# Performance work log

Hardware: AMD Instinct MI355X
Metric: run time of the kernel (lower is better)

Reference implementation:

```python
import jax, jax.numpy as jnp
import numpy as np

N = 100000   # number of website nodes
E = 800000   # edges per edge type
F = 128      # in_feats == out_feats
NEG_SLOPE = 0.2


def setup_inputs() -> dict:
    key = jax.random.key(0)
    ks = jax.random.split(key, 16)
    s = 1.0 / np.sqrt(F)
    return {
        "feat": jax.random.normal(ks[0], (N, F), jnp.float32),
        "src_u": jax.random.randint(ks[1], (E,), 0, N),
        "dst_u": jax.random.randint(ks[2], (E,), 0, N),
        "src_r": jax.random.randint(ks[3], (E,), 0, N),
        "dst_r": jax.random.randint(ks[4], (E,), 0, N),
        # fc_self (no bias)
        "W_self": jax.random.uniform(ks[5], (F, F), jnp.float32, -s, s),
        # attn branch 'user'
        "W_u": jax.random.uniform(ks[6], (F, F), jnp.float32, -s, s),
        "a_l_u": jax.random.uniform(ks[7], (F,), jnp.float32, -s, s),
        "a_r_u": jax.random.uniform(ks[8], (F,), jnp.float32, -s, s),
        # attn branch 'reuse'
        "W_r": jax.random.uniform(ks[9], (F, F), jnp.float32, -s, s),
        "a_l_r": jax.random.uniform(ks[10], (F,), jnp.float32, -s, s),
        "a_r_r": jax.random.uniform(ks[11], (F,), jnp.float32, -s, s),
        # fc_neigh (with bias)
        "W_neigh": jax.random.uniform(ks[12], (F, F), jnp.float32, -s, s),
        "b_neigh": jax.random.uniform(ks[13], (F,), jnp.float32, -s, s),
        # module-level bias parameter
        "bias": jnp.zeros((F,), jnp.float32),
    }


def _attn_aggregate(feat, W, a_l, a_r, src, dst, n_nodes):
    """GAT-style single-head aggregation over one edge type.
    Returns [n_nodes, F] = sum_{e: dst(e)=v} softmax_v(leaky_relu(el[src]+er[dst])) * h[src]."""
    h = feat @ W                                    # [N, F] (feat_src == feat_dst)
    el = h @ a_l                                    # [N]
    er = h @ a_r                                    # [N]
    e = jax.nn.leaky_relu(el[src] + er[dst], NEG_SLOPE)   # [E]
    # edge_softmax: normalize over incoming edges of each dst node
    m = jax.ops.segment_max(e, dst, num_segments=n_nodes)  # [N] (-inf for isolated dst, unused)
    ex = jnp.exp(e - m[dst])                        # [E]
    denom = jax.ops.segment_sum(ex, dst, num_segments=n_nodes)  # [N]
    a = ex / denom[dst]                             # [E]
    msg = h[src] * a[:, None]                       # [E, F]
    return jax.ops.segment_sum(msg, dst, num_segments=n_nodes)  # [N, F]


def reference(feat, src_u, dst_u, src_r, dst_r, W_self, W_u, a_l_u, a_r_u,
              W_r, a_l_r, a_r_r, W_neigh, b_neigh, bias):
    n = feat.shape[0]
    neigh_u = _attn_aggregate(feat, W_u, a_l_u, a_r_u, src_u, dst_u, n)
    neigh_r = _attn_aggregate(feat, W_r, a_l_r, a_r_r, src_r, dst_r, n)
    # multi_update_all cross reducer 'mean' over the two edge types
    neigh = 0.5 * (neigh_u + neigh_r)
    h_neigh = neigh @ W_neigh + b_neigh             # fc_neigh
    rst = feat @ W_self + h_neigh                   # fc_self(h_self) + h_neigh
    return rst + bias
```

## Files before the change

### kernel.cpp

```cpp
#include <hip/hip_runtime.h>

#define F 128
#define NEG_SLOPE 0.2f
#define SHIFT 9
#define BPB 512
#define NBS 512

typedef _Float16 f16_t;
typedef _Float16 f16x8 __attribute__((ext_vector_type(8)));
typedef _Float16 f16x2 __attribute__((ext_vector_type(2)));
typedef float f32x4 __attribute__((ext_vector_type(4)));

__global__ __launch_bounds__(128) void prep_mats(
    const float* __restrict__ Wu, const float* __restrict__ Wr,
    const float* __restrict__ Ws, const float* __restrict__ Wn,
    const float* __restrict__ alu, const float* __restrict__ aru,
    const float* __restrict__ alr, const float* __restrict__ arr_,
    f16_t* __restrict__ Mtu, f16_t* __restrict__ Mtr, f16_t* __restrict__ Wts,
    float* __restrict__ wlu, float* __restrict__ wru,
    float* __restrict__ wlr, float* __restrict__ wrr)
{
    int b = blockIdx.x;
    int tid = threadIdx.x;
    if (b < 256) {
        int k = b & 127;
        const float* W = (b < 128) ? Wu : Wr;
        f16_t* M = (b < 128) ? Mtu : Mtr;
        float acc = 0.f;
        for (int t = 0; t < F; t++) acc += W[k * F + t] * Wn[t * F + tid];
        M[tid * F + k] = (f16_t)acc;
    } else if (b < 384) {
        int c = b - 256;
        Wts[c * F + tid] = (f16_t)Ws[tid * F + c];
    } else {
        int which = b - 384;
        const float* W = (which < 2) ? Wu : Wr;
        const float* a = (which == 0) ? alu : (which == 1) ? aru : (which == 2) ? alr : arr_;
        float acc = 0.f;
        for (int c = 0; c < F; c++) acc += W[tid * F + c] * a[c];
        float* o = (which == 0) ? wlu : (which == 1) ? wru : (which == 2) ? wlr : wrr;
        o[tid] = acc;
    }
}


__global__ __launch_bounds__(256) void cast_p1a(
    const float* __restrict__ feat,
    const float* __restrict__ wlu, const float* __restrict__ wru,
    const float* __restrict__ wlr, const float* __restrict__ wrr,
    f16_t* __restrict__ featb,
    float* __restrict__ elu, float* __restrict__ eru,
    float* __restrict__ elr, float* __restrict__ err_,
    const int* __restrict__ dst_u, const int* __restrict__ dst_r,
    int* __restrict__ cnt_bb,
    int Eu, int Et, int N, int chunk, int n, int nbk)
{
    int b = blockIdx.x;
    int tid = threadIdx.x;
    if (b < 256) {
        __shared__ int hist[NBS];
        for (int i = tid; i < NBS; i += 256) hist[i] = 0;
        __syncthreads();
        int e0 = b * chunk;
        int e1 = e0 + chunk; if (e1 > Et) e1 = Et;
        int u1 = (e1 < Eu) ? e1 : Eu;
        for (int e = e0 + tid; e < u1; e += 256) {
            int bin = dst_u[e];
            atomicAdd(&hist[bin >> SHIFT], 1);
        }
        int r0 = (e0 > Eu) ? e0 : Eu;
        for (int e = r0 + tid; e < e1; e += 256) {
            int bin = N + dst_r[e - Eu];
            atomicAdd(&hist[bin >> SHIFT], 1);
        }
        __syncthreads();
        for (int i = tid; i < NBS; i += 256) cnt_bb[b * NBS + i] = hist[i];
        return;
    }
    int fid = b - 256;
    int lane = tid & 63;
    int wave = tid >> 6;
    int lo = lane & 15, hi = lane >> 4;
    int base = fid * 64 + wave * 16;
    if (base >= n) return;
    int row = base + lo;
    if (row > n - 1) row = n - 1;
    const float* fp = feat + (size_t)row * F + hi * 8;
    f16_t* fb = featb + (size_t)row * F + hi * 8;
    const float* wsel = (lo == 0) ? wlu : (lo == 1) ? wru : (lo == 2) ? wlr : wrr;

    f32x4 acc = (f32x4){0.f, 0.f, 0.f, 0.f};
#pragma unroll
    for (int ks = 0; ks < 4; ks++) {
        float4 a0 = *(const float4*)(fp + ks * 32);
        float4 a1 = *(const float4*)(fp + ks * 32 + 4);
        f16x8 af;
        af[0] = (f16_t)a0.x; af[1] = (f16_t)a0.y; af[2] = (f16_t)a0.z; af[3] = (f16_t)a0.w;
        af[4] = (f16_t)a1.x; af[5] = (f16_t)a1.y; af[6] = (f16_t)a1.z; af[7] = (f16_t)a1.w;
        *(f16x8*)(fb + ks * 32) = af;
        f16x8 bf;
#pragma unroll
        for (int q = 0; q < 8; q++) bf[q] = (f16_t)0;
        if (lo < 4) {
            float4 b0 = *(const float4*)(wsel + ks * 32 + hi * 8);
            float4 b1 = *(const float4*)(wsel + ks * 32 + hi * 8 + 4);
            bf[0] = (f16_t)b0.x; bf[1] = (f16_t)b0.y; bf[2] = (f16_t)b0.z; bf[3] = (f16_t)b0.w;
            bf[4] = (f16_t)b1.x; bf[5] = (f16_t)b1.y; bf[6] = (f16_t)b1.z; bf[7] = (f16_t)b1.w;
        }
        acc = __builtin_amdgcn_mfma_f32_16x16x32_f16(af, bf, acc, 0, 0, 0);
    }
    if (lo < 4) {
        float* oarr = (lo == 0) ? elu : (lo == 1) ? eru : (lo == 2) ? elr : err_;
#pragma unroll
        for (int j = 0; j < 4; j++) {
            int r = base + hi * 4 + j;
            if (r < n) oarr[r] = acc[j];
        }
    }
}


__global__ __launch_bounds__(256) void scan_bb1(int* __restrict__ cnt_bb,
                                                int* __restrict__ btot, int nbk)
{
    int k = blockIdx.x;
    int tid = threadIdx.x;
    __shared__ int lds[256];
    int v = cnt_bb[tid * NBS + k];
    lds[tid] = v;
    __syncthreads();
    for (int off = 1; off < 256; off <<= 1) {
        int add = (tid >= off) ? lds[tid - off] : 0;
        __syncthreads();
        lds[tid] += add;
        __syncthreads();
    }
    cnt_bb[tid * NBS + k] = lds[tid] - v;
    if (tid == 255) btot[k] = lds[255];
}

__global__ __launch_bounds__(512) void scan_bb2(const int* __restrict__ btot,
                                                int* __restrict__ bbase,
                                                int* __restrict__ rp,
                                                int nbk, int twoN, int Et)
{
    __shared__ int lds[512];
    int t = threadIdx.x;
    int v = (t < nbk) ? btot[t] : 0;
    lds[t] = v;
    __syncthreads();
    for (int off = 1; off < 512; off <<= 1) {
        int add = (t >= off) ? lds[t - off] : 0;
        __syncthreads();
        lds[t] += add;
        __syncthreads();
    }
    bbase[t] = lds[t] - v;
    if (t == 0) rp[twoN] = Et;
}


__global__ __launch_bounds__(256) void p1b_scatter(
    const int* __restrict__ src_u, const int* __restrict__ dst_u,
    const int* __restrict__ src_r, const int* __restrict__ dst_r,
    const int* __restrict__ cnt_bb, const int* __restrict__ bbase,
    uint2* __restrict__ bucketed,
    int Eu, int Et, int N, int chunk, int nbk)
{
    int b = blockIdx.x;
    int tid = threadIdx.x;
    __shared__ int cur[NBS];
    for (int i = tid; i < nbk; i += 256) cur[i] = bbase[i] + cnt_bb[b * NBS + i];
    __syncthreads();
    int e0 = b * chunk;
    int e1 = e0 + chunk; if (e1 > Et) e1 = Et;
    int u1 = (e1 < Eu) ? e1 : Eu;
    for (int e = e0 + tid; e < u1; e += 256) {
        int bin = dst_u[e];
        int s = src_u[e];
        int pos = atomicAdd(&cur[bin >> SHIFT], 1);
        bucketed[pos] = make_uint2((unsigned)s, (unsigned)bin);
    }
    int r0 = (e0 > Eu) ? e0 : Eu;
    for (int e = r0 + tid; e < e1; e += 256) {
        int bin = N + dst_r[e - Eu];
        int s = src_r[e - Eu];
        int pos = atomicAdd(&cur[bin >> SHIFT], 1);
        bucketed[pos] = make_uint2((unsigned)s, (unsigned)bin);
    }
}


__global__ __launch_bounds__(256) void p2_build(
    const uint2* __restrict__ bucketed, const int* __restrict__ bbase,
    int* __restrict__ rp, int* __restrict__ csr, int twoN)
{
    int k = blockIdx.x;
    int tid = threadIdx.x;
    int beg = bbase[k], end = bbase[k + 1];
    __shared__ int hist[BPB];
    __shared__ int psum[256];
    for (int i = tid; i < BPB; i += 256) hist[i] = 0;
    __syncthreads();
    for (int i = beg + tid; i < end; i += 256) {
        uint2 p = bucketed[i];
        atomicAdd(&hist[p.y & (BPB - 1)], 1);
    }
    __syncthreads();
    int a0 = hist[2 * tid], a1 = hist[2 * tid + 1];
    psum[tid] = a0 + a1;
    __syncthreads();
    for (int off = 1; off < 256; off <<= 1) {
        int add = (tid >= off) ? psum[tid - off] : 0;
        __syncthreads();
        psum[tid] += add;
        __syncthreads();
    }
    int base0 = beg + psum[tid] - (a0 + a1);
    int bin0 = (k << SHIFT) + 2 * tid;
    if (bin0 < twoN)     rp[bin0]     = base0;
    if (bin0 + 1 < twoN) rp[bin0 + 1] = base0 + a0;
    __syncthreads();
    hist[2 * tid]     = base0;
    hist[2 * tid + 1] = base0 + a0;
    __syncthreads();
    for (int i = beg + tid; i < end; i += 256) {
        uint2 p = bucketed[i];
        int pos = atomicAdd(&hist[p.y & (BPB - 1)], 1);
        csr[pos] = (int)p.x;
    }
}


__global__ __launch_bounds__(256) void aggregate_fused(
    const f16_t* __restrict__ featb,
    const float* __restrict__ elu, const float* __restrict__ eru,
    const float* __restrict__ elr, const float* __restrict__ err_,
    const int* __restrict__ rp, const int* __restrict__ csr,
    f16_t* __restrict__ aggu, f16_t* __restrict__ aggr, int n)
{
    int wid = (int)(((size_t)blockIdx.x * 256 + threadIdx.x) >> 6);
    if (wid >= n) return;
    int lane = threadIdx.x & 63;
    int g = lane >> 4, lo = lane & 15;

    int begu = rp[wid],     endu = rp[wid + 1];
    int begr = rp[n + wid], endr = rp[n + wid + 1];
    float ervu = eru[wid];
    float ervr = err_[wid];

    union UP { f16x2 h; int i; };
    union UV { f16x8 v; f16x2 p[4]; };

    f16x2 z = {(f16_t)0, (f16_t)0};
    f16x2 au0 = z, au1 = z, au2 = z, au3 = z;
    f16x2 ar0 = z, ar1 = z, ar2 = z, ar3 = z;
    float du = 0.f, dr = 0.f;

    int iu = begu + g, ir = begr + g;

    int cu0 = (iu     < endu) ? csr[iu]     : -1;
    int cu1 = (iu + 4 < endu) ? csr[iu + 4] : -1;
    int cr0 = (ir     < endr) ? csr[ir]     : -1;
    int cr1 = (ir + 4 < endr) ? csr[ir + 4] : -1;
    UV hu0, hu1, hr0, hr1;
    hu0.v = *(const f16x8*)&featb[(size_t)(cu0 < 0 ? 0 : cu0) * F + lo * 8];
    hu1.v = *(const f16x8*)&featb[(size_t)(cu1 < 0 ? 0 : cu1) * F + lo * 8];
    hr0.v = *(const f16x8*)&featb[(size_t)(cr0 < 0 ? 0 : cr0) * F + lo * 8];
    hr1.v = *(const f16x8*)&featb[(size_t)(cr1 < 0 ? 0 : cr1) * F + lo * 8];
    float eu0 = elu[cu0 < 0 ? 0 : cu0];
    float eu1 = elu[cu1 < 0 ? 0 : cu1];
    float er0 = elr[cr0 < 0 ? 0 : cr0];
    float er1 = elr[cr1 < 0 ? 0 : cr1];

    while (iu < endu || ir < endr) {
        int nu0 = (iu + 8  < endu) ? csr[iu + 8]  : -1;
        int nu1 = (iu + 12 < endu) ? csr[iu + 12] : -1;
        int nr0 = (ir + 8  < endr) ? csr[ir + 8]  : -1;
        int nr1 = (ir + 12 < endr) ? csr[ir + 12] : -1;
        UV pu0, pu1, pr0, pr1;
        pu0.v = *(const f16x8*)&featb[(size_t)(nu0 < 0 ? 0 : nu0) * F + lo * 8];
        pu1.v = *(const f16x8*)&featb[(size_t)(nu1 < 0 ? 0 : nu1) * F + lo * 8];
        pr0.v = *(const f16x8*)&featb[(size_t)(nr0 < 0 ? 0 : nr0) * F + lo * 8];
        pr1.v = *(const f16x8*)&featb[(size_t)(nr1 < 0 ? 0 : nr1) * F + lo * 8];
        float fu0 = elu[nu0 < 0 ? 0 : nu0];
        float fu1 = elu[nu1 < 0 ? 0 : nu1];
        float fr0 = elr[nr0 < 0 ? 0 : nr0];
        float fr1 = elr[nr1 < 0 ? 0 : nr1];

        {
            float e = eu0 + ervu; e = fmaxf(e, NEG_SLOPE * e);
            float ex = (cu0 >= 0) ? __expf(e) : 0.f;
            f16_t exh = (f16_t)ex; f16x2 exv = {exh, exh};
            au0 += exv * hu0.p[0]; au1 += exv * hu0.p[1];
            au2 += exv * hu0.p[2]; au3 += exv * hu0.p[3];
            du += ex;
        }
        {
            float e = eu1 + ervu; e = fmaxf(e, NEG_SLOPE * e);
            float ex = (cu1 >= 0) ? __expf(e) : 0.f;
            f16_t exh = (f16_t)ex; f16x2 exv = {exh, exh};
            au0 += exv * hu1.p[0]; au1 += exv * hu1.p[1];
            au2 += exv * hu1.p[2]; au3 += exv * hu1.p[3];
            du += ex;
        }
        {
            float e = er0 + ervr; e = fmaxf(e, NEG_SLOPE * e);
            float ex = (cr0 >= 0) ? __expf(e) : 0.f;
            f16_t exh = (f16_t)ex; f16x2 exv = {exh, exh};
            ar0 += exv * hr0.p[0]; ar1 += exv * hr0.p[1];
            ar2 += exv * hr0.p[2]; ar3 += exv * hr0.p[3];
            dr += ex;
        }
        {
            float e = er1 + ervr; e = fmaxf(e, NEG_SLOPE * e);
            float ex = (cr1 >= 0) ? __expf(e) : 0.f;
            f16_t exh = (f16_t)ex; f16x2 exv = {exh, exh};
            ar0 += exv * hr1.p[0]; ar1 += exv * hr1.p[1];
            ar2 += exv * hr1.p[2]; ar3 += exv * hr1.p[3];
            dr += ex;
        }

        hu0 = pu0; hu1 = pu1; hr0 = pr0; hr1 = pr1;
        eu0 = fu0; eu1 = fu1; er0 = fr0; er1 = fr1;
        cu0 = nu0; cu1 = nu1; cr0 = nr0; cr1 = nr1;
        iu += 8; ir += 8;
    }

#pragma unroll
    for (int off = 16; off < 64; off <<= 1) {
        du += __shfl_xor(du, off);
        dr += __shfl_xor(dr, off);
        UP x;
        x.h = au0; x.i = __shfl_xor(x.i, off); au0 += x.h;
        x.h = au1; x.i = __shfl_xor(x.i, off); au1 += x.h;
        x.h = au2; x.i = __shfl_xor(x.i, off); au2 += x.h;
        x.h = au3; x.i = __shfl_xor(x.i, off); au3 += x.h;
        x.h = ar0; x.i = __shfl_xor(x.i, off); ar0 += x.h;
        x.h = ar1; x.i = __shfl_xor(x.i, off); ar1 += x.h;
        x.h = ar2; x.i = __shfl_xor(x.i, off); ar2 += x.h;
        x.h = ar3; x.i = __shfl_xor(x.i, off); ar3 += x.h;
    }

    if (g == 0) {
        float invu = (du > 0.f) ? 0.5f / du : 0.f;
        float invr = (dr > 0.f) ? 0.5f / dr : 0.f;
        f16_t ihu = (f16_t)invu, ihr = (f16_t)invr;
        f16x2 ivu = {ihu, ihu}, ivr = {ihr, ihr};
        UV ou, orr;
        ou.p[0] = au0 * ivu; ou.p[1] = au1 * ivu; ou.p[2] = au2 * ivu; ou.p[3] = au3 * ivu;
        orr.p[0] = ar0 * ivr; orr.p[1] = ar1 * ivr; orr.p[2] = ar2 * ivr; orr.p[3] = ar3 * ivr;
        *(f16x8*)&aggu[(size_t)wid * F + lo * 8] = ou.v;
        *(f16x8*)&aggr[(size_t)wid * F + lo * 8] = orr.v;
    }
}


__global__ __launch_bounds__(1024) void mfma_final3(
    const f16_t* __restrict__ featb,
    const f16_t* __restrict__ aggu, const f16_t* __restrict__ aggr,
    const f16_t* __restrict__ Wts, const f16_t* __restrict__ Mtu,
    const f16_t* __restrict__ Mtr,
    const float* __restrict__ bn, const float* __restrict__ bias,
    float* __restrict__ out, int n, int ntiles)
{
    __shared__ f16_t Ls[F * F];
    __shared__ f16_t Lu[F * F];
    __shared__ f16_t Lr[F * F];
    for (int i = threadIdx.x; i < 2048; i += 1024) {
        int c = i >> 4, kc = i & 15, kcs = kc ^ (c & 15);
        *(f16x8*)&Ls[c * F + kcs * 8] = *(const f16x8*)&Wts[c * F + kc * 8];
        *(f16x8*)&Lu[c * F + kcs * 8] = *(const f16x8*)&Mtu[c * F + kc * 8];
        *(f16x8*)&Lr[c * F + kcs * 8] = *(const f16x8*)&Mtr[c * F + kc * 8];
    }
    __syncthreads();

    int lane = threadIdx.x & 63;
    int wave = threadIdx.x >> 6;
    int lo = lane & 15, hi = lane >> 4;

    float cb[8];
#pragma unroll
    for (int t = 0; t < 8; t++) cb[t] = bn[t * 16 + lo] + bias[t * 16 + lo];

    for (int tile = blockIdx.x; tile < ntiles; tile += 256) {
        int row0 = tile * 256 + wave * 16;
        if (row0 >= n) continue;
        int arow = row0 + lo;
        if (arow > n - 1) arow = n - 1;
        const f16_t* pf = featb + (size_t)arow * F + hi * 8;
        const f16_t* pu = aggu + (size_t)arow * F + hi * 8;
        const f16_t* pr = aggr + (size_t)arow * F + hi * 8;

        f32x4 acc[8];
#pragma unroll
        for (int t = 0; t < 8; t++) acc[t] = (f32x4){0.f, 0.f, 0.f, 0.f};

#pragma unroll
        for (int ks = 0; ks < 4; ks++) {
            f16x8 a1 = *(const f16x8*)(pf + ks * 32);
            f16x8 a2 = *(const f16x8*)(pu + ks * 32);
            f16x8 a3 = *(const f16x8*)(pr + ks * 32);
#pragma unroll
            for (int t = 0; t < 8; t++) {
                int c = t * 16 + lo;
                int kcs = (ks * 4 + hi) ^ lo;
                f16x8 bs = *(const f16x8*)&Ls[c * F + kcs * 8];
                f16x8 bu = *(const f16x8*)&Lu[c * F + kcs * 8];
                f16x8 br = *(const f16x8*)&Lr[c * F + kcs * 8];
                acc[t] = __builtin_amdgcn_mfma_f32_16x16x32_f16(a1, bs, acc[t], 0, 0, 0);
                acc[t] = __builtin_amdgcn_mfma_f32_16x16x32_f16(a2, bu, acc[t], 0, 0, 0);
                acc[t] = __builtin_amdgcn_mfma_f32_16x16x32_f16(a3, br, acc[t], 0, 0, 0);
            }
        }

#pragma unroll
        for (int j = 0; j < 4; j++) {
            int r = row0 + hi * 4 + j;
            if (r < n) {
                float* op = out + (size_t)r * F + lo;
#pragma unroll
                for (int t = 0; t < 8; t++) op[t * 16] = acc[t][j] + cb[t];
            }
        }
    }
}


extern "C" void kernel_launch(void* const* d_in, const int* in_sizes, int n_in,
                              void* d_out, int out_size, void* d_ws, size_t ws_size,
                              hipStream_t stream) {
    const float* feat   = (const float*)d_in[0];
    const int*   src_u  = (const int*)d_in[1];
    const int*   dst_u  = (const int*)d_in[2];
    const int*   src_r  = (const int*)d_in[3];
    const int*   dst_r  = (const int*)d_in[4];
    const float* W_self = (const float*)d_in[5];
    const float* W_u    = (const float*)d_in[6];
    const float* a_l_u  = (const float*)d_in[7];
    const float* a_r_u  = (const float*)d_in[8];
    const float* W_r    = (const float*)d_in[9];
    const float* a_l_r  = (const float*)d_in[10];
    const float* a_r_r  = (const float*)d_in[11];
    const float* W_ngh  = (const float*)d_in[12];
    const float* b_ngh  = (const float*)d_in[13];
    const float* bias   = (const float*)d_in[14];
    float* out = (float*)d_out;

    const int N  = in_sizes[0] / F;
    const int Eu = in_sizes[1];
    const int Er = in_sizes[3];
    const int Et = Eu + Er;
    const int twoN = 2 * N;
    const int nbk = (twoN + BPB - 1) >> SHIFT;

    char* ws = (char*)d_ws;
    size_t off = 0;
    auto alloc = [&](size_t bytes) -> void* {
        void* p = ws + off;
        off = (off + bytes + 255) & ~(size_t)255;
        return p;
    };
    f16_t* featb = (f16_t*)alloc((size_t)N * F * 2);
    f16_t* aggu  = (f16_t*)alloc((size_t)N * F * 2);
    f16_t* aggr  = (f16_t*)alloc((size_t)N * F * 2);
    f16_t* Mt_u  = (f16_t*)alloc((size_t)F * F * 2);
    f16_t* Mt_r  = (f16_t*)alloc((size_t)F * F * 2);
    f16_t* Wt_s  = (f16_t*)alloc((size_t)F * F * 2);
    float* wlu = (float*)alloc((size_t)F * 4);
    float* wru = (float*)alloc((size_t)F * 4);
    float* wlr = (float*)alloc((size_t)F * 4);
    float* wrr = (float*)alloc((size_t)F * 4);
    float* elu = (float*)alloc((size_t)N * 4);
    float* eru = (float*)alloc((size_t)N * 4);
    float* elr = (float*)alloc((size_t)N * 4);
    float* err_ = (float*)alloc((size_t)N * 4);
    int* cnt_bb = (int*)alloc((size_t)256 * NBS * 4);
    int* btot   = (int*)alloc((size_t)NBS * 4);
    int* bbase  = (int*)alloc((size_t)(NBS + 1) * 4);
    int* rp2    = (int*)alloc(((size_t)twoN + 1) * 4);
    uint2* bucketed = (uint2*)alloc((size_t)Et * 8);
    int* csr2   = (int*)alloc((size_t)Et * 4);

    prep_mats<<<388, 128, 0, stream>>>(W_u, W_r, W_self, W_ngh,
                                       a_l_u, a_r_u, a_l_r, a_r_r,
                                       Mt_u, Mt_r, Wt_s, wlu, wru, wlr, wrr);

    const int chunk = (Et + 255) / 256;
    int castBlocks = (N + 63) / 64;
    cast_p1a<<<256 + castBlocks, 256, 0, stream>>>(
        feat, wlu, wru, wlr, wrr, featb, elu, eru, elr, err_,
        dst_u, dst_r, cnt_bb, Eu, Et, N, chunk, N, nbk);

    scan_bb1<<<nbk, 256, 0, stream>>>(cnt_bb, btot, nbk);
    scan_bb2<<<1, 512, 0, stream>>>(btot, bbase, rp2, nbk, twoN, Et);
    p1b_scatter<<<256, 256, 0, stream>>>(src_u, dst_u, src_r, dst_r,
                                         cnt_bb, bbase, bucketed,
                                         Eu, Et, N, chunk, nbk);
    p2_build<<<nbk, 256, 0, stream>>>(bucketed, bbase, rp2, csr2, twoN);

    aggregate_fused<<<(N + 3) / 4, 256, 0, stream>>>(featb, elu, eru, elr, err_,
                                                     rp2, csr2, aggu, aggr, N);
    int ntiles = (N + 255) / 256;
    mfma_final3<<<256, 1024, 0, stream>>>(featb, aggu, aggr,
                                          Wt_s, Mt_u, Mt_r,
                                          b_ngh, bias, out, N, ntiles);
}
```

Baseline: 154.1 us.

## Pack bucketed edges into 32 bits and sort CSR neighbors by source octant

The bucketed edge array is packed as a 17-bit source id plus a 9-bit local destination bin in one 32-bit word, halving that intermediate's memory traffic. p2_build now keeps a histogram with 8 sub-bins per destination keyed by the source's high bits. Each node's CSR neighbor list therefore comes out roughly grouped by source range, which should improve locality of the feature gathers in aggregation. The cost is an 8x larger shared-memory histogram, and the 17-bit packing only holds while N stays under 131072.

```diff
diff --git a/kernel.cpp b/kernel.cpp
--- a/kernel.cpp
+++ b/kernel.cpp
@@ -5,6 +5,7 @@
 #define SHIFT 9
 #define BPB 512
 #define NBS 512
+#define OCTSH 14
 
 typedef _Float16 f16_t;
 typedef _Float16 f16x8 __attribute__((ext_vector_type(8)));
@@ -164,7 +165,7 @@
     const int* __restrict__ src_u, const int* __restrict__ dst_u,
     const int* __restrict__ src_r, const int* __restrict__ dst_r,
     const int* __restrict__ cnt_bb, const int* __restrict__ bbase,
-    uint2* __restrict__ bucketed,
+    unsigned* __restrict__ bucketed,
     int Eu, int Et, int N, int chunk, int nbk)
 {
     int b = blockIdx.x;
@@ -179,36 +180,41 @@
         int bin = dst_u[e];
         int s = src_u[e];
         int pos = atomicAdd(&cur[bin >> SHIFT], 1);
-        bucketed[pos] = make_uint2((unsigned)s, (unsigned)bin);
+        bucketed[pos] = (unsigned)s | ((unsigned)(bin & (BPB - 1)) << 17);
     }
     int r0 = (e0 > Eu) ? e0 : Eu;
     for (int e = r0 + tid; e < e1; e += 256) {
         int bin = N + dst_r[e - Eu];
         int s = src_r[e - Eu];
         int pos = atomicAdd(&cur[bin >> SHIFT], 1);
-        bucketed[pos] = make_uint2((unsigned)s, (unsigned)bin);
+        bucketed[pos] = (unsigned)s | ((unsigned)(bin & (BPB - 1)) << 17);
     }
 }
 
 
 __global__ __launch_bounds__(256) void p2_build(
-    const uint2* __restrict__ bucketed, const int* __restrict__ bbase,
+    const unsigned* __restrict__ bucketed, const int* __restrict__ bbase,
     int* __restrict__ rp, int* __restrict__ csr, int twoN)
 {
     int k = blockIdx.x;
     int tid = threadIdx.x;
     int beg = bbase[k], end = bbase[k + 1];
-    __shared__ int hist[BPB];
+    __shared__ int hist[BPB * 8];
     __shared__ int psum[256];
-    for (int i = tid; i < BPB; i += 256) hist[i] = 0;
+#pragma unroll
+    for (int i = tid; i < BPB * 8; i += 256) hist[i] = 0;
     __syncthreads();
     for (int i = beg + tid; i < end; i += 256) {
-        uint2 p = bucketed[i];
-        atomicAdd(&hist[p.y & (BPB - 1)], 1);
-    }
-    __syncthreads();
-    int a0 = hist[2 * tid], a1 = hist[2 * tid + 1];
-    psum[tid] = a0 + a1;
+        unsigned w = bucketed[i];
+        int src = (int)(w & 0x1FFFF);
+        int binlow = (int)((w >> 17) & (BPB - 1));
+        atomicAdd(&hist[(binlow << 3) | (src >> OCTSH)], 1);
+    }
+    __syncthreads();
+    int s = 0;
+#pragma unroll
+    for (int i = 0; i < 16; i++) s += hist[tid * 16 + i];
+    psum[tid] = s;
     __syncthreads();
     for (int off = 1; off < 256; off <<= 1) {
         int add = (tid >= off) ? psum[tid - off] : 0;
@@ -216,18 +222,25 @@
         psum[tid] += add;
         __syncthreads();
     }
-    int base0 = beg + psum[tid] - (a0 + a1);
-    int bin0 = (k << SHIFT) + 2 * tid;
-    if (bin0 < twoN)     rp[bin0]     = base0;
-    if (bin0 + 1 < twoN) rp[bin0 + 1] = base0 + a0;
-    __syncthreads();
-    hist[2 * tid]     = base0;
-    hist[2 * tid + 1] = base0 + a0;
+    int run = beg + psum[tid] - s;
+#pragma unroll
+    for (int i = 0; i < 16; i++) {
+        int c = tid * 16 + i;
+        int v = hist[c];
+        hist[c] = run;
+        if ((c & 7) == 0) {
+            int bin0 = (k << SHIFT) + (c >> 3);
+            if (bin0 < twoN) rp[bin0] = run;
+        }
+        run += v;
+    }
     __syncthreads();
     for (int i = beg + tid; i < end; i += 256) {
-        uint2 p = bucketed[i];
-        int pos = atomicAdd(&hist[p.y & (BPB - 1)], 1);
-        csr[pos] = (int)p.x;
+        unsigned w = bucketed[i];
+        int src = (int)(w & 0x1FFFF);
+        int binlow = (int)((w >> 17) & (BPB - 1));
+        int pos = atomicAdd(&hist[(binlow << 3) | (src >> OCTSH)], 1);
+        csr[pos] = src;
     }
 }
 
@@ -479,7 +492,7 @@
     int* btot   = (int*)alloc((size_t)NBS * 4);
     int* bbase  = (int*)alloc((size_t)(NBS + 1) * 4);
     int* rp2    = (int*)alloc(((size_t)twoN + 1) * 4);
-    uint2* bucketed = (uint2*)alloc((size_t)Et * 8);
+    unsigned* bucketed = (unsigned*)alloc((size_t)Et * 4);
     int* csr2   = (int*)alloc((size_t)Et * 4);
 
     prep_mats<<<388, 128, 0, stream>>>(W_u, W_r, W_self, W_ngh,
```

Result: no change. 155.9 us (+1.2%).
